# Kernel tuning notes

Measured on AMD Instinct MI355X. Metric: run time of the kernel, lower is better.

Reference implementation:

```python
import jax, jax.numpy as jnp
import numpy as np

N = 100000   # nodes
E = 1600000  # edges
IN = 512     # in_channels
H = 256      # hidden_channels
C = 40       # out_channels
BITS = 8     # INT8 fake quantization


def fake_quant(x, bits=BITS):
    """Symmetric per-tensor quantize-dequantize with straight-through estimator."""
    qmax = float(2 ** (bits - 1) - 1)
    scale = jnp.max(jnp.abs(x)) / qmax + 1e-12
    q = jnp.clip(jnp.round(x / scale), -qmax - 1.0, qmax) * scale
    # STE: forward = q, backward = identity
    return x + jax.lax.stop_gradient(q - x)


def quant_linear(x, w, b):
    # LinearQuantized: fake-quant inputs and weights, fp accumulate
    return fake_quant(x) @ fake_quant(w).T + b


def gcn_propagate(x, edge_index):
    """Symmetric-normalized sparse propagation: out = D^-1/2 A D^-1/2 x."""
    src, dst = edge_index[0], edge_index[1]
    deg = jax.ops.segment_sum(jnp.ones((E,), x.dtype), dst, num_segments=N)
    dinv = jnp.where(deg > 0, jax.lax.rsqrt(jnp.maximum(deg, 1.0)), 0.0)
    coef = dinv[src] * dinv[dst]                     # [E]
    msgs = x[src] * coef[:, None]                    # [E, C]
    return jax.ops.segment_sum(msgs, dst, num_segments=N)  # [N, C]


def setup_inputs() -> dict:
    key = jax.random.key(0)
    ks = jax.random.split(key, 6)
    x = jax.random.normal(ks[0], (N, IN), jnp.float32)
    edge_index = jax.random.randint(ks[1], (2, E), 0, N, dtype=jnp.int32)
    w1 = jax.random.normal(ks[2], (H, IN), jnp.float32) * (1.0 / np.sqrt(IN))
    b1 = jnp.zeros((H,), jnp.float32)
    w2 = jax.random.normal(ks[3], (C, H), jnp.float32) * (1.0 / np.sqrt(H))
    b2 = jnp.zeros((C,), jnp.float32)
    return {"x": x, "edge_index": edge_index, "w1": w1, "b1": b1, "w2": w2, "b2": b2}


def reference(x, edge_index, w1, b1, w2, b2):
    # dropout: identity in eval mode
    h = jax.nn.relu(quant_linear(x, w1, b1))         # [N, H]
    z = quant_linear(h, w2, b2)                      # [N, C]
    z = gcn_propagate(z, edge_index)                 # [N, C]
    return jax.nn.log_softmax(z, axis=1)
```

## Files before the change

kernel.cpp:

```cpp
#include <hip/hip_runtime.h>
#include <hip/hip_bf16.h>
#include <hip/hip_fp16.h>
#include <stdint.h>
#include <stddef.h>

#define NN   100000
#define NE   1600000
#define INC  512
#define HID  256
#define OC   40
#define OCP  48

#define LDS1 144
#define LDSB2 272

#define NBKT ((NN + 255) / 256)
#define NMT1 ((NN + 127) / 128)
#define GEMM1_BLKS (((NMT1 + 7) / 8) * 16)

#define ABS_X_BLKS  2048
#define ABS_W1_BLKS 128
#define ABS_W2_BLKS 16
#define ABS_TOT     (ABS_X_BLKS + ABS_W1_BLKS + ABS_W2_BLKS)
#define CHIST_BLKS  256
#define QX_BLKS     3200
#define QW1_BLKS    128
#define QW2_BLKS    16
#define BIN_BLOCKS  400
#define BIN_EPB     (NE / BIN_BLOCKS)
#define L3_QW1_BASE QX_BLKS
#define L3_QW2_BASE (QX_BLKS + QW1_BLKS)
#define L3_BIN_BASE (QX_BLKS + QW1_BLKS + QW2_BLKS)

typedef float  f32x4  __attribute__((ext_vector_type(4)));
typedef int    i32x4  __attribute__((ext_vector_type(4)));
typedef _Float16 f16x8 __attribute__((ext_vector_type(8)));

__device__ unsigned g_amax_bits[4];
__device__ float    g_dinv[NN];
__device__ signed char g_qx[(size_t)NN * INC];
__device__ signed char g_qw1[HID * INC];
__device__ signed char g_qw2[OCP * HID];
__device__ _Float16 g_h[(size_t)NN * HID];
__device__ float    g_z[(size_t)NN * OC];
__device__ unsigned g_chist[NBKT];
__device__ unsigned g_cstart[NBKT + 1];
__device__ unsigned g_ccur[NBKT];
__device__ uint2    g_bin[NE];
__device__ unsigned g_rowstart[NN + 1];
__device__ int      g_csr_src[NE];

__device__ __forceinline__ float quantf(float v, float rs) {
    return fminf(fmaxf(rintf(v * rs), -128.0f), 127.0f);
}
__device__ __forceinline__ int pack4(float a, float b, float c, float d, float rs) {
    int q0 = (int)quantf(a, rs), q1 = (int)quantf(b, rs);
    int q2 = (int)quantf(c, rs), q3 = (int)quantf(d, rs);
    return (q0 & 255) | ((q1 & 255) << 8) | ((q2 & 255) << 16) | ((q3 & 255) << 24);
}

__global__ void init_kernel() {
    int idx = blockIdx.x * blockDim.x + threadIdx.x;
    int stride = gridDim.x * blockDim.x;
    for (int i = idx; i < NBKT; i += stride) g_chist[i] = 0u;
    for (int i = idx; i < (OCP * HID) / 4; i += stride) ((int*)g_qw2)[i] = 0;
    if (idx < 4) g_amax_bits[idx] = 0u;
}

__global__ void __launch_bounds__(256) absmax_chist_kernel(const float* __restrict__ x,
                                                           const float* __restrict__ w1,
                                                           const float* __restrict__ w2,
                                                           const int* __restrict__ ei) {
    __shared__ unsigned shist[NBKT];
    __shared__ float sm[4];
    int b = blockIdx.x;
    int t = threadIdx.x;
    if (b < ABS_TOT) {
        const float* src; int n4, slot, bbase, nb;
        if (b < ABS_X_BLKS) {
            src = x;  n4 = (NN * INC) / 4;  slot = 0; bbase = 0;                       nb = ABS_X_BLKS;
        } else if (b < ABS_X_BLKS + ABS_W1_BLKS) {
            src = w1; n4 = (HID * INC) / 4; slot = 1; bbase = ABS_X_BLKS;              nb = ABS_W1_BLKS;
        } else {
            src = w2; n4 = (OC * HID) / 4;  slot = 2; bbase = ABS_X_BLKS + ABS_W1_BLKS; nb = ABS_W2_BLKS;
        }
        int idx = (b - bbase) * 256 + t;
        int stride = nb * 256;
        const f32x4* s4 = (const f32x4*)src;
        float m = 0.0f;
        for (int i = idx; i < n4; i += stride) {
            f32x4 v = s4[i];
            m = fmaxf(m, fmaxf(fmaxf(fabsf(v.x), fabsf(v.y)),
                               fmaxf(fabsf(v.z), fabsf(v.w))));
        }
#pragma unroll
        for (int off = 32; off > 0; off >>= 1) m = fmaxf(m, __shfl_xor(m, off, 64));
        if ((t & 63) == 0) sm[t >> 6] = m;
        __syncthreads();
        if (t == 0) {
            float mm = fmaxf(fmaxf(sm[0], sm[1]), fmaxf(sm[2], sm[3]));
            atomicMax(&g_amax_bits[slot], __float_as_uint(mm));
        }
    } else {
        const int* dst = ei + NE;
        for (int i = t; i < NBKT; i += 256) shist[i] = 0u;
        __syncthreads();
        int idx = (b - ABS_TOT) * 256 + t;
        int stride = CHIST_BLKS * 256;
        for (int e = idx; e < NE; e += stride) atomicAdd(&shist[dst[e] >> 8], 1u);
        __syncthreads();
        for (int i = t; i < NBKT; i += 256) {
            unsigned c = shist[i];
            if (c) atomicAdd(&g_chist[i], c);
        }
    }
}

__global__ void cscan_kernel() {
    int t = threadIdx.x;
    unsigned v = (t < NBKT) ? g_chist[t] : 0u;
    int lane = t & 63, wv = t >> 6;
    unsigned sc = v;
#pragma unroll
    for (int off = 1; off < 64; off <<= 1) {
        unsigned n = __shfl_up(sc, off, 64);
        if (lane >= off) sc += n;
    }
    __shared__ unsigned ws[8];
    if (lane == 63) ws[wv] = sc;
    __syncthreads();
    unsigned woff = 0;
    for (int w = 0; w < 8; w++) if (w < wv) woff += ws[w];
    unsigned excl = woff + sc - v;
    if (t < NBKT) { g_cstart[t] = excl; g_ccur[t] = excl; }
    if (t == 0) g_cstart[NBKT] = NE;
}

__global__ void __launch_bounds__(256) quant_bin_kernel(const float* __restrict__ x,
                                                        const float* __restrict__ w1,
                                                        const float* __restrict__ w2,
                                                        const int* __restrict__ ei) {
    __shared__ unsigned hist[NBKT];
    __shared__ unsigned base[NBKT];
    int b = blockIdx.x;
    int t = threadIdx.x;
    if (b < QX_BLKS) {
        float rs = 1.0f / (__uint_as_float(g_amax_bits[0]) / 127.0f + 1e-12f);
        int idx = b * 256 + t;
        int stride = QX_BLKS * 256;
        int n16 = (NN * INC) / 16;
        i32x4* d = (i32x4*)g_qx;
        for (int i = idx; i < n16; i += stride) {
            const f32x4* s = (const f32x4*)(x + (size_t)i * 16);
            f32x4 v0 = s[0], v1 = s[1], v2 = s[2], v3 = s[3];
            i32x4 o;
            o[0] = pack4(v0.x, v0.y, v0.z, v0.w, rs);
            o[1] = pack4(v1.x, v1.y, v1.z, v1.w, rs);
            o[2] = pack4(v2.x, v2.y, v2.z, v2.w, rs);
            o[3] = pack4(v3.x, v3.y, v3.z, v3.w, rs);
            d[i] = o;
        }
    } else if (b < L3_BIN_BASE) {
        const float* src; int* dst; int nint, slot, bbase, nb;
        if (b < L3_QW2_BASE) { src = w1; dst = (int*)g_qw1; nint = (HID * INC) / 4; slot = 1; bbase = L3_QW1_BASE; nb = QW1_BLKS; }
        else                 { src = w2; dst = (int*)g_qw2; nint = (OC * HID) / 4;  slot = 2; bbase = L3_QW2_BASE; nb = QW2_BLKS; }
        float rs = 1.0f / (__uint_as_float(g_amax_bits[slot]) / 127.0f + 1e-12f);
        int idx = (b - bbase) * 256 + t;
        int stride = nb * 256;
        for (int i = idx; i < nint; i += stride) {
            f32x4 v = *(const f32x4*)(src + (size_t)i * 4);
            dst[i] = pack4(v.x, v.y, v.z, v.w, rs);
        }
    } else {
        const int* srcp = ei;
        const int* dstp = ei + NE;
        int bb = b - L3_BIN_BASE;
        int e0 = bb * BIN_EPB, e1 = e0 + BIN_EPB;
        for (int i = t; i < NBKT; i += 256) hist[i] = 0u;
        __syncthreads();
        for (int e = e0 + t; e < e1; e += 256) atomicAdd(&hist[dstp[e] >> 8], 1u);
        __syncthreads();
        for (int i = t; i < NBKT; i += 256) {
            unsigned c = hist[i];
            base[i] = c ? atomicAdd(&g_ccur[i], c) : 0u;
            hist[i] = 0u;
        }
        __syncthreads();
        for (int e = e0 + t; e < e1; e += 256) {
            int d = dstp[e], s = srcp[e];
            int bk = d >> 8;
            unsigned r = atomicAdd(&hist[bk], 1u);
            g_bin[base[bk] + r] = make_uint2((unsigned)s, (unsigned)d);
        }
    }
}

__global__ void __launch_bounds__(256) gemm1_local_kernel(const float* __restrict__ b1) {
    __shared__ char lA[2][128 * LDS1];
    __shared__ char lB[2][128 * LDS1];
    int t = threadIdx.x;
    if (blockIdx.x >= GEMM1_BLKS) {
        int b = blockIdx.x - GEMM1_BLKS;
        unsigned* hist = (unsigned*)lA;
        unsigned* curs = hist + 256;
        unsigned* wsum = curs + 256;
        unsigned e0 = g_cstart[b], e1 = g_cstart[b + 1];
        hist[t] = 0u;
        __syncthreads();
        for (unsigned e = e0 + t; e < e1; e += 256) atomicAdd(&hist[g_bin[e].y & 255], 1u);
        __syncthreads();
        unsigned v = hist[t];
        int lane = t & 63, wv = t >> 6;
        unsigned sc = v;
#pragma unroll
        for (int off = 1; off < 64; off <<= 1) {
            unsigned n = __shfl_up(sc, off, 64);
            if (lane >= off) sc += n;
        }
        if (lane == 63) wsum[wv] = sc;
        __syncthreads();
        unsigned woff = 0;
        for (int w = 0; w < 4; w++) if (w < wv) woff += wsum[w];
        unsigned excl = woff + sc - v;
        int node = b * 256 + t;
        if (node < NN) {
            g_rowstart[node] = e0 + excl;
            g_dinv[node] = v ? rsqrtf((float)v) : 0.0f;
        }
        if (b == 0 && t == 0) g_rowstart[NN] = NE;
        curs[t] = excl;
        __syncthreads();
        for (unsigned e = e0 + t; e < e1; e += 256) {
            uint2 ed = g_bin[e];
            unsigned r = atomicAdd(&curs[ed.y & 255], 1u);
            g_csr_src[e0 + r] = (int)ed.x;
        }
        return;
    }
    int group = blockIdx.x >> 4;
    int ntile = (blockIdx.x >> 3) & 1;
    int mtile = group * 8 + (blockIdx.x & 7);
    if (mtile >= NMT1) return;
    int lane = t & 63, wv = t >> 6;
    int quad = lane >> 4, l16 = lane & 15;
    int mq = wv >> 1, nq = wv & 1;

    int srow = t >> 3;
    int sch  = t & 7;

    const signed char* xb[4];
    const signed char* wb[4];
#pragma unroll
    for (int p = 0; p < 4; p++) {
        int gr = mtile * 128 + p * 32 + srow; if (gr >= NN) gr = NN - 1;
        xb[p] = g_qx + (size_t)gr * INC + sch * 16;
        wb[p] = g_qw1 + (size_t)(ntile * 128 + p * 32 + srow) * INC + sch * 16;
    }

    i32x4 av[4], bv[4];
#pragma unroll
    for (int p = 0; p < 4; p++) {
        av[p] = *(const i32x4*)(xb[p]);
        bv[p] = *(const i32x4*)(wb[p]);
    }

    i32x4 acc[4][4] = {};
#pragma unroll 1
    for (int kit = 0; kit < 4; kit++) {
        int bs = kit & 1;
#pragma unroll
        for (int p = 0; p < 4; p++) {
            int row = p * 32 + srow;
            *(i32x4*)(lA[bs] + row * LDS1 + sch * 16) = av[p];
            *(i32x4*)(lB[bs] + row * LDS1 + sch * 16) = bv[p];
        }
        if (kit + 1 < 4) {
#pragma unroll
            for (int p = 0; p < 4; p++) {
                av[p] = *(const i32x4*)(xb[p] + (kit + 1) * 128);
                bv[p] = *(const i32x4*)(wb[p] + (kit + 1) * 128);
            }
        }
        __syncthreads();
#pragma unroll
        for (int ks = 0; ks < 2; ks++) {
            int cs = ks * 64 + quad * 16;
            i32x4 a[4], b[4];
#pragma unroll
            for (int i = 0; i < 4; i++)
                a[i] = *(const i32x4*)(lA[bs] + (mq * 64 + i * 16 + l16) * LDS1 + cs);
#pragma unroll
            for (int j = 0; j < 4; j++)
                b[j] = *(const i32x4*)(lB[bs] + (nq * 64 + j * 16 + l16) * LDS1 + cs);
#pragma unroll
            for (int i = 0; i < 4; i++)
#pragma unroll
                for (int j = 0; j < 4; j++)
                    acc[i][j] = __builtin_amdgcn_mfma_i32_16x16x64_i8(a[i], b[j], acc[i][j], 0, 0, 0);
        }
    }
    float s = (__uint_as_float(g_amax_bits[0]) / 127.0f + 1e-12f)
            * (__uint_as_float(g_amax_bits[1]) / 127.0f + 1e-12f);
    float lmax = 0.0f;
#pragma unroll
    for (int j = 0; j < 4; j++) {
        int col = ntile * 128 + nq * 64 + j * 16 + l16;
        float bias = b1[col];
#pragma unroll
        for (int i = 0; i < 4; i++) {
#pragma unroll
            for (int r = 0; r < 4; r++) {
                int grow = mtile * 128 + mq * 64 + i * 16 + quad * 4 + r;
                float v = fmaxf(s * (float)acc[i][j][r] + bias, 0.0f);
                lmax = fmaxf(lmax, v);
                if (grow < NN) g_h[(size_t)grow * HID + col] = (_Float16)v;
            }
        }
    }
#pragma unroll
    for (int off = 32; off > 0; off >>= 1) lmax = fmaxf(lmax, __shfl_xor(lmax, off, 64));
    if (lane == 0) atomicMax(&g_amax_bits[3], __float_as_uint(lmax));
}

__launch_bounds__(256)
__global__ void gemm2_kernel(const float* __restrict__ b2) {
    __shared__ char lB2[OCP * LDSB2];
    __shared__ char lA2[128 * LDS1];
    int t = threadIdx.x;
    int mtile = blockIdx.x;
    int lane = t & 63, wv = t >> 6;
    int quad = lane >> 4, l16 = lane & 15;

#pragma unroll
    for (int p = 0; p < 3; p++) {
        int ci = p * 256 + t;
        int row = ci >> 4, ch = ci & 15;
        *(i32x4*)(lB2 + row * LDSB2 + ch * 16) =
            *(const i32x4*)(g_qw2 + row * 256 + ch * 16);
    }

    float scale_h = __uint_as_float(g_amax_bits[3]) / 127.0f + 1e-12f;
    float rs = 1.0f / scale_h;
    int srow = t >> 3, sch = t & 7;
    const _Float16* hbase[4];
#pragma unroll
    for (int p = 0; p < 4; p++) {
        int gr = mtile * 128 + p * 32 + srow; if (gr >= NN) gr = NN - 1;
        hbase[p] = g_h + (size_t)gr * HID + sch * 16;
    }

    i32x4 acc[2][3] = {};
#pragma unroll 1
    for (int kit = 0; kit < 2; kit++) {
        if (kit) __syncthreads();
#pragma unroll
        for (int p = 0; p < 4; p++) {
            int row = p * 32 + srow;
            const _Float16* hp = hbase[p] + kit * 128;
            f16x8 v0 = *(const f16x8*)(hp);
            f16x8 v1 = *(const f16x8*)(hp + 8);
            i32x4 o;
            o[0] = pack4((float)v0[0], (float)v0[1], (float)v0[2], (float)v0[3], rs);
            o[1] = pack4((float)v0[4], (float)v0[5], (float)v0[6], (float)v0[7], rs);
            o[2] = pack4((float)v1[0], (float)v1[1], (float)v1[2], (float)v1[3], rs);
            o[3] = pack4((float)v1[4], (float)v1[5], (float)v1[6], (float)v1[7], rs);
            *(i32x4*)(lA2 + row * LDS1 + sch * 16) = o;
        }
        __syncthreads();
#pragma unroll
        for (int ks = 0; ks < 2; ks++) {
            int cs = ks * 64 + quad * 16;
            i32x4 a[2], b[3];
#pragma unroll
            for (int i = 0; i < 2; i++)
                a[i] = *(const i32x4*)(lA2 + (wv * 32 + i * 16 + l16) * LDS1 + cs);
#pragma unroll
            for (int j = 0; j < 3; j++)
                b[j] = *(const i32x4*)(lB2 + (j * 16 + l16) * LDSB2 + kit * 128 + cs);
#pragma unroll
            for (int i = 0; i < 2; i++)
#pragma unroll
                for (int j = 0; j < 3; j++)
                    acc[i][j] = __builtin_amdgcn_mfma_i32_16x16x64_i8(a[i], b[j], acc[i][j], 0, 0, 0);
        }
    }
    float s = scale_h * (__uint_as_float(g_amax_bits[2]) / 127.0f + 1e-12f);
#pragma unroll
    for (int j = 0; j < 3; j++) {
        int col = j * 16 + l16;
        float bias = (col < OC) ? b2[col] : 0.0f;
#pragma unroll
        for (int i = 0; i < 2; i++) {
#pragma unroll
            for (int r = 0; r < 4; r++) {
                int grow = mtile * 128 + wv * 32 + i * 16 + quad * 4 + r;
                if (col < OC && grow < NN)
                    g_z[(size_t)grow * OC + col] = s * (float)acc[i][j][r] + bias;
            }
        }
    }
}

__launch_bounds__(256)
__global__ void gather_kernel(float* __restrict__ out) {
    int node = (blockIdx.x * 256 + threadIdx.x) >> 6;
    int lane = threadIdx.x & 63;
    if (node >= NN) return;
    unsigned e0 = g_rowstart[node], e1 = g_rowstart[node + 1];
    float dinvd = g_dinv[node];
    bool ch = (lane < OC);
    float acc0 = 0.0f, acc1 = 0.0f;
    unsigned e = e0;
    for (; e + 8 <= e1; e += 8) {
        int s0 = g_csr_src[e],     s1 = g_csr_src[e + 1];
        int s2 = g_csr_src[e + 2], s3 = g_csr_src[e + 3];
        int s4 = g_csr_src[e + 4], s5 = g_csr_src[e + 5];
        int s6 = g_csr_src[e + 6], s7 = g_csr_src[e + 7];
        float c0 = g_dinv[s0], c1 = g_dinv[s1], c2 = g_dinv[s2], c3 = g_dinv[s3];
        float c4 = g_dinv[s4], c5 = g_dinv[s5], c6 = g_dinv[s6], c7 = g_dinv[s7];
        float z0 = ch ? g_z[(size_t)s0 * OC + lane] : 0.0f;
        float z1 = ch ? g_z[(size_t)s1 * OC + lane] : 0.0f;
        float z2 = ch ? g_z[(size_t)s2 * OC + lane] : 0.0f;
        float z3 = ch ? g_z[(size_t)s3 * OC + lane] : 0.0f;
        float z4 = ch ? g_z[(size_t)s4 * OC + lane] : 0.0f;
        float z5 = ch ? g_z[(size_t)s5 * OC + lane] : 0.0f;
        float z6 = ch ? g_z[(size_t)s6 * OC + lane] : 0.0f;
        float z7 = ch ? g_z[(size_t)s7 * OC + lane] : 0.0f;
        acc0 += (z0 * c0 + z1 * c1) + (z2 * c2 + z3 * c3);
        acc1 += (z4 * c4 + z5 * c5) + (z6 * c6 + z7 * c7);
    }
    for (; e + 4 <= e1; e += 4) {
        int s0 = g_csr_src[e],     s1 = g_csr_src[e + 1];
        int s2 = g_csr_src[e + 2], s3 = g_csr_src[e + 3];
        float c0 = g_dinv[s0], c1 = g_dinv[s1], c2 = g_dinv[s2], c3 = g_dinv[s3];
        float z0 = ch ? g_z[(size_t)s0 * OC + lane] : 0.0f;
        float z1 = ch ? g_z[(size_t)s1 * OC + lane] : 0.0f;
        float z2 = ch ? g_z[(size_t)s2 * OC + lane] : 0.0f;
        float z3 = ch ? g_z[(size_t)s3 * OC + lane] : 0.0f;
        acc0 += (z0 * c0 + z1 * c1) + (z2 * c2 + z3 * c3);
    }
    for (; e < e1; e++) {
        int s0 = g_csr_src[e];
        float z0 = ch ? g_z[(size_t)s0 * OC + lane] : 0.0f;
        acc1 += z0 * g_dinv[s0];
    }
    float acc = (acc0 + acc1) * dinvd;
    float m = ch ? acc : -1e30f;
#pragma unroll
    for (int off = 32; off > 0; off >>= 1) m = fmaxf(m, __shfl_xor(m, off, 64));
    float ex = ch ? __expf(acc - m) : 0.0f;
    float ssum = ex;
#pragma unroll
    for (int off = 32; off > 0; off >>= 1) ssum += __shfl_xor(ssum, off, 64);
    float lg = __logf(ssum);
    if (ch) out[(size_t)node * OC + lane] = acc - m - lg;
}

extern "C" void kernel_launch(void* const* d_in, const int* in_sizes, int n_in,
                              void* d_out, int out_size, void* d_ws, size_t ws_size,
                              hipStream_t stream) {
    const float* x  = (const float*)d_in[0];
    const int*   ei = (const int*)d_in[1];
    const float* w1 = (const float*)d_in[2];
    const float* b1 = (const float*)d_in[3];
    const float* w2 = (const float*)d_in[4];
    const float* b2 = (const float*)d_in[5];
    float* out = (float*)d_out;
    (void)d_ws; (void)ws_size; (void)in_sizes; (void)n_in; (void)out_size;

    init_kernel<<<64, 256, 0, stream>>>();
    absmax_chist_kernel<<<ABS_TOT + CHIST_BLKS, 256, 0, stream>>>(x, w1, w2, ei);
    cscan_kernel<<<1, 512, 0, stream>>>();
    quant_bin_kernel<<<L3_BIN_BASE + BIN_BLOCKS, 256, 0, stream>>>(x, w1, w2, ei);
    gemm1_local_kernel<<<GEMM1_BLKS + NBKT, 256, 0, stream>>>(b1);
    gemm2_kernel<<<(NN + 127) / 128, 256, 0, stream>>>(b2);
    gather_kernel<<<(NN + 3) / 4, 256, 0, stream>>>(out);
}
```

Baseline: 560.2 us.

## Fuse input int8 quantization into GEMM1 operand loads, drop the quantized-x buffer

Removes the separate pass that quantized x to an int8 global buffer and instead quantizes fp32 x on the fly while loading GEMM1 tiles into registers. This avoids writing and rereading the int8 copy of x. In exchange, GEMM1 reads fp32 data, four times the bytes of int8, and x is read by both column tiles, relying on cache for reuse. Register pressure and conversion work inside the GEMM also increase.

```diff
diff --git a/kernel.cpp b/kernel.cpp
--- a/kernel.cpp
+++ b/kernel.cpp
@@ -23,14 +23,11 @@
 #define ABS_W2_BLKS 16
 #define ABS_TOT     (ABS_X_BLKS + ABS_W1_BLKS + ABS_W2_BLKS)
 #define CHIST_BLKS  256
-#define QX_BLKS     3200
 #define QW1_BLKS    128
 #define QW2_BLKS    16
+#define QW_TOT      (QW1_BLKS + QW2_BLKS)
 #define BIN_BLOCKS  400
 #define BIN_EPB     (NE / BIN_BLOCKS)
-#define L3_QW1_BASE QX_BLKS
-#define L3_QW2_BASE (QX_BLKS + QW1_BLKS)
-#define L3_BIN_BASE (QX_BLKS + QW1_BLKS + QW2_BLKS)
 
 typedef float  f32x4  __attribute__((ext_vector_type(4)));
 typedef int    i32x4  __attribute__((ext_vector_type(4)));
@@ -38,7 +35,6 @@
 
 __device__ unsigned g_amax_bits[4];
 __device__ float    g_dinv[NN];
-__device__ signed char g_qx[(size_t)NN * INC];
 __device__ signed char g_qw1[HID * INC];
 __device__ signed char g_qw2[OCP * HID];
 __device__ _Float16 g_h[(size_t)NN * HID];
@@ -57,6 +53,18 @@
     int q0 = (int)quantf(a, rs), q1 = (int)quantf(b, rs);
     int q2 = (int)quantf(c, rs), q3 = (int)quantf(d, rs);
     return (q0 & 255) | ((q1 & 255) << 8) | ((q2 & 255) << 16) | ((q3 & 255) << 24);
+}
+__device__ __forceinline__ i32x4 loadpack16(const float* p, float rs) {
+    f32x4 v0 = *(const f32x4*)(p);
+    f32x4 v1 = *(const f32x4*)(p + 4);
+    f32x4 v2 = *(const f32x4*)(p + 8);
+    f32x4 v3 = *(const f32x4*)(p + 12);
+    i32x4 o;
+    o[0] = pack4(v0.x, v0.y, v0.z, v0.w, rs);
+    o[1] = pack4(v1.x, v1.y, v1.z, v1.w, rs);
+    o[2] = pack4(v2.x, v2.y, v2.z, v2.w, rs);
+    o[3] = pack4(v3.x, v3.y, v3.z, v3.w, rs);
+    return o;
 }
 
 __global__ void init_kernel() {
@@ -136,34 +144,17 @@
     if (t == 0) g_cstart[NBKT] = NE;
 }
 
-__global__ void __launch_bounds__(256) quant_bin_kernel(const float* __restrict__ x,
-                                                        const float* __restrict__ w1,
+__global__ void __launch_bounds__(256) quant_bin_kernel(const float* __restrict__ w1,
                                                         const float* __restrict__ w2,
                                                         const int* __restrict__ ei) {
     __shared__ unsigned hist[NBKT];
     __shared__ unsigned base[NBKT];
     int b = blockIdx.x;
     int t = threadIdx.x;
-    if (b < QX_BLKS) {
-        float rs = 1.0f / (__uint_as_float(g_amax_bits[0]) / 127.0f + 1e-12f);
-        int idx = b * 256 + t;
-        int stride = QX_BLKS * 256;
-        int n16 = (NN * INC) / 16;
-        i32x4* d = (i32x4*)g_qx;
-        for (int i = idx; i < n16; i += stride) {
-            const f32x4* s = (const f32x4*)(x + (size_t)i * 16);
-            f32x4 v0 = s[0], v1 = s[1], v2 = s[2], v3 = s[3];
-            i32x4 o;
-            o[0] = pack4(v0.x, v0.y, v0.z, v0.w, rs);
-            o[1] = pack4(v1.x, v1.y, v1.z, v1.w, rs);
-            o[2] = pack4(v2.x, v2.y, v2.z, v2.w, rs);
-            o[3] = pack4(v3.x, v3.y, v3.z, v3.w, rs);
-            d[i] = o;
-        }
-    } else if (b < L3_BIN_BASE) {
+    if (b < QW_TOT) {
         const float* src; int* dst; int nint, slot, bbase, nb;
-        if (b < L3_QW2_BASE) { src = w1; dst = (int*)g_qw1; nint = (HID * INC) / 4; slot = 1; bbase = L3_QW1_BASE; nb = QW1_BLKS; }
-        else                 { src = w2; dst = (int*)g_qw2; nint = (OC * HID) / 4;  slot = 2; bbase = L3_QW2_BASE; nb = QW2_BLKS; }
+        if (b < QW1_BLKS) { src = w1; dst = (int*)g_qw1; nint = (HID * INC) / 4; slot = 1; bbase = 0;        nb = QW1_BLKS; }
+        else              { src = w2; dst = (int*)g_qw2; nint = (OC * HID) / 4;  slot = 2; bbase = QW1_BLKS; nb = QW2_BLKS; }
         float rs = 1.0f / (__uint_as_float(g_amax_bits[slot]) / 127.0f + 1e-12f);
         int idx = (b - bbase) * 256 + t;
         int stride = nb * 256;
@@ -174,7 +165,7 @@
     } else {
         const int* srcp = ei;
         const int* dstp = ei + NE;
-        int bb = b - L3_BIN_BASE;
+        int bb = b - QW_TOT;
         int e0 = bb * BIN_EPB, e1 = e0 + BIN_EPB;
         for (int i = t; i < NBKT; i += 256) hist[i] = 0u;
         __syncthreads();
@@ -195,7 +186,8 @@
     }
 }
 
-__global__ void __launch_bounds__(256) gemm1_local_kernel(const float* __restrict__ b1) {
+__global__ void __launch_bounds__(256) gemm1_local_kernel(const float* __restrict__ x,
+                                                          const float* __restrict__ b1) {
     __shared__ char lA[2][128 * LDS1];
     __shared__ char lB[2][128 * LDS1];
     int t = threadIdx.x;
@@ -248,19 +240,21 @@
     int srow = t >> 3;
     int sch  = t & 7;
 
-    const signed char* xb[4];
+    float rsx = 1.0f / (__uint_as_float(g_amax_bits[0]) / 127.0f + 1e-12f);
+
+    const float* xb[4];
     const signed char* wb[4];
 #pragma unroll
     for (int p = 0; p < 4; p++) {
         int gr = mtile * 128 + p * 32 + srow; if (gr >= NN) gr = NN - 1;
-        xb[p] = g_qx + (size_t)gr * INC + sch * 16;
+        xb[p] = x + (size_t)gr * INC + sch * 16;
         wb[p] = g_qw1 + (size_t)(ntile * 128 + p * 32 + srow) * INC + sch * 16;
     }
 
     i32x4 av[4], bv[4];
 #pragma unroll
     for (int p = 0; p < 4; p++) {
-        av[p] = *(const i32x4*)(xb[p]);
+        av[p] = loadpack16(xb[p], rsx);
         bv[p] = *(const i32x4*)(wb[p]);
     }
 
@@ -277,7 +271,7 @@
         if (kit + 1 < 4) {
 #pragma unroll
             for (int p = 0; p < 4; p++) {
-                av[p] = *(const i32x4*)(xb[p] + (kit + 1) * 128);
+                av[p] = loadpack16(xb[p] + (kit + 1) * 128, rsx);
                 bv[p] = *(const i32x4*)(wb[p] + (kit + 1) * 128);
             }
         }
@@ -471,8 +465,8 @@
     init_kernel<<<64, 256, 0, stream>>>();
     absmax_chist_kernel<<<ABS_TOT + CHIST_BLKS, 256, 0, stream>>>(x, w1, w2, ei);
     cscan_kernel<<<1, 512, 0, stream>>>();
-    quant_bin_kernel<<<L3_BIN_BASE + BIN_BLOCKS, 256, 0, stream>>>(x, w1, w2, ei);
-    gemm1_local_kernel<<<GEMM1_BLKS + NBKT, 256, 0, stream>>>(b1);
+    quant_bin_kernel<<<QW_TOT + BIN_BLOCKS, 256, 0, stream>>>(w1, w2, ei);
+    gemm1_local_kernel<<<GEMM1_BLKS + NBKT, 256, 0, stream>>>(x, b1);
     gemm2_kernel<<<(NN + 127) / 128, 256, 0, stream>>>(b2);
     gather_kernel<<<(NN + 3) / 4, 256, 0, stream>>>(out);
 }
```

Result: faster. 546.3 us (-2.5%).
